# Optimization experiments

Hardware: AMD Instinct MI355X
Metric: run time of the kernel (lower is better)

## Reference

```python
import jax, jax.numpy as jnp
import numpy as np

SCORE_THR = 0.05
IOU_THR = 0.5
TOPK = 1000  # per-class candidate cap (static shape for jit)


def _make_anchors(img):
    """RetinaNet anchors: 9 per location over P3-P7 (strides 8..128)."""
    strides = [8, 16, 32, 64, 128]
    sizes = [32, 64, 128, 256, 512]
    ratios = [0.5, 1.0, 2.0]
    scales = [2.0 ** 0, 2.0 ** (1.0 / 3.0), 2.0 ** (2.0 / 3.0)]
    out = []
    for stride, size in zip(strides, sizes):
        ws, hs = [], []
        for r in ratios:
            for sc in scales:
                a = (size * sc) ** 2
                w = np.sqrt(a / r)
                ws.append(w)
                hs.append(w * r)
        ws = np.asarray(ws)
        hs = np.asarray(hs)
        fs = img // stride
        c = (np.arange(fs) + 0.5) * stride
        cy, cx = np.meshgrid(c, c, indexing='ij')
        cx = cx.reshape(-1)[:, None]
        cy = cy.reshape(-1)[:, None]
        boxes = np.stack([cx - ws / 2, cy - hs / 2, cx + ws / 2, cy + hs / 2], axis=-1)
        out.append(boxes.reshape(-1, 4))
    return np.concatenate(out, axis=0).astype(np.float32)


def setup_inputs() -> dict:
    key = jax.random.key(0)
    k1, k2 = jax.random.split(key)
    img = 1024
    anchors = jnp.asarray(_make_anchors(img))          # [196416, 4]
    A = anchors.shape[0]
    cls_heads = jax.random.uniform(k1, (1, A, 80), dtype=jnp.float32)   # post-sigmoid probs
    reg_heads = jax.random.normal(k2, (1, A, 4), dtype=jnp.float32)
    return {"cls_heads": cls_heads, "reg_heads": reg_heads, "anchors": anchors,
            "img_h": img, "img_w": img}


def _decode(anchors, deltas):
    # BBoxTransform: std = [0.1, 0.1, 0.2, 0.2]
    w = anchors[:, 2] - anchors[:, 0]
    h = anchors[:, 3] - anchors[:, 1]
    cx = anchors[:, 0] + 0.5 * w
    cy = anchors[:, 1] + 0.5 * h
    dx = deltas[:, 0] * 0.1
    dy = deltas[:, 1] * 0.1
    dw = deltas[:, 2] * 0.2
    dh = deltas[:, 3] * 0.2
    pcx = cx + dx * w
    pcy = cy + dy * h
    pw = jnp.exp(dw) * w
    ph = jnp.exp(dh) * h
    return jnp.stack([pcx - 0.5 * pw, pcy - 0.5 * ph,
                      pcx + 0.5 * pw, pcy + 0.5 * ph], axis=-1)


def _iou(b):  # [K,4] -> [K,K]
    area = jnp.maximum(b[:, 2] - b[:, 0], 0) * jnp.maximum(b[:, 3] - b[:, 1], 0)
    lt = jnp.maximum(b[:, None, :2], b[None, :, :2])
    rb = jnp.minimum(b[:, None, 2:], b[None, :, 2:])
    wh = jnp.maximum(rb - lt, 0.0)
    inter = wh[..., 0] * wh[..., 1]
    union = area[:, None] + area[None, :] - inter
    return inter / jnp.maximum(union, 1e-8)


def _nms_one_class(scores_c, boxes):
    # threshold, take top-K candidates (static shape), greedy NMS
    masked = jnp.where(scores_c > SCORE_THR, scores_c, -1.0)
    _, idx = jax.lax.top_k(masked, TOPK)
    s = scores_c[idx]                       # [K]
    b = boxes[idx]                          # [K,4]
    valid = s > SCORE_THR
    iou = _iou(b)                           # [K,K]
    rng = jnp.arange(TOPK)

    def body(i, keep):
        sup = (iou[i] > IOU_THR) & (rng > i) & keep[i]
        return keep & ~sup

    keep = jax.lax.fori_loop(0, TOPK, body, valid)
    return jnp.where(keep, s, 0.0), jnp.where(keep[:, None], b, 0.0), keep


def reference(cls_heads, reg_heads, anchors, img_h, img_w):
    # batch = 1 (the torch code squeezes the batch dim)
    scores_ac = cls_heads[0]                # [A, C]
    deltas = reg_heads[0]                   # [A, 4]
    boxes = _decode(anchors, deltas)        # [A, 4]
    # ClipBoxes
    boxes = jnp.stack([
        jnp.clip(boxes[:, 0], 0.0, img_w),
        jnp.clip(boxes[:, 1], 0.0, img_h),
        jnp.clip(boxes[:, 2], 0.0, img_w),
        jnp.clip(boxes[:, 3], 0.0, img_h)], axis=-1)
    scores_ca = scores_ac.T                 # [C, A]
    s, b, keep = jax.vmap(_nms_one_class, in_axes=(0, None))(scores_ca, boxes)
    C = scores_ca.shape[0]
    cls_idx = jnp.where(keep, jnp.arange(C)[:, None], -1)
    # padded, static-shape equivalent of (finalScores, finalAnchorBoxesIndexes,
    # finalAnchorBoxesCoordinates); invalid slots have score 0 / class -1
    return s.reshape(-1), cls_idx.reshape(-1), b.reshape(-1, 4)
```

## Files before the change

kernel.cpp:

```cpp
#include <hip/hip_runtime.h>
#include <hip/hip_bf16.h>
#include <math.h>

typedef unsigned long long u64;
typedef unsigned int u32;

#define C_NUM 80
#define TOPK 1000
#define CAP 2048
#define HB 128
#define STG 32
#define NCHUNK 16
#define SCORE_THR 0.05f
#define IOU_THR 0.5f
#define GRID_SCAN 256

__device__ __forceinline__ float exp_cr(float x) {
    return (float)exp((double)x);
}

__device__ __forceinline__ void decode_box(const float* __restrict__ anch,
                                           const float* __restrict__ reg,
                                           int a, float fw, float fh, float4* out) {
#pragma clang fp contract(off)
    float a0 = anch[(size_t)a * 4 + 0], a1 = anch[(size_t)a * 4 + 1];
    float a2 = anch[(size_t)a * 4 + 2], a3 = anch[(size_t)a * 4 + 3];
    float d0 = reg[(size_t)a * 4 + 0], d1 = reg[(size_t)a * 4 + 1];
    float d2 = reg[(size_t)a * 4 + 2], d3 = reg[(size_t)a * 4 + 3];
    float w = a2 - a0, h = a3 - a1;
    float cx = a0 + 0.5f * w, cy = a1 + 0.5f * h;
    float dx = d0 * 0.1f, dy = d1 * 0.1f, dw = d2 * 0.2f, dh = d3 * 0.2f;
    float t1 = dx * w; float pcx = cx + t1;
    float t2 = dy * h; float pcy = cy + t2;
    float pw = exp_cr(dw) * w;
    float ph = exp_cr(dh) * h;
    float x1 = pcx - 0.5f * pw, y1 = pcy - 0.5f * ph;
    float x2 = pcx + 0.5f * pw, y2 = pcy + 0.5f * ph;
    x1 = fminf(fmaxf(x1, 0.0f), fw);
    y1 = fminf(fmaxf(y1, 0.0f), fh);
    x2 = fminf(fmaxf(x2, 0.0f), fw);
    y2 = fminf(fmaxf(y2, 0.0f), fh);
    *out = make_float4(x1, y1, x2, y2);
}

__global__ __launch_bounds__(1024)
void hist_kernel(const float4* __restrict__ cls4, u32* __restrict__ slices, int nvec) {
    __shared__ u32 h[C_NUM * HB];
    int tid = threadIdx.x;
    for (int i = tid; i < C_NUM * HB; i += 1024) h[i] = 0u;
    __syncthreads();
    int gid = blockIdx.x * 1024 + tid;
    const int stride = GRID_SCAN * 1024;
    const int dC = (stride * 4) % C_NUM;
    int c0 = (gid * 4) % C_NUM;
    for (int v = gid; v < nvec; v += stride) {
        float4 f = cls4[v];
        float e[4] = {f.x, f.y, f.z, f.w};
        int cc = c0;
#pragma unroll
        for (int k = 0; k < 4; ++k) {
            int t = (((int)__float_as_uint(e[k])) - 0x3F000000) >> 16;
            if (t > 0) {
                t = t > HB - 1 ? HB - 1 : t;
                atomicAdd(&h[cc * HB + t], 1u);
            }
            cc++; if (cc == C_NUM) cc = 0;
        }
        c0 += dC; if (c0 >= C_NUM) c0 -= C_NUM;
    }
    __syncthreads();
    u32* my = slices + (size_t)blockIdx.x * (C_NUM * HB);
    for (int i = tid; i < C_NUM * HB; i += 1024) my[i] = h[i];
}

__global__ __launch_bounds__(1024)
void thr_kernel(const u32* __restrict__ slices, u32* __restrict__ thrG) {
    __shared__ u32 part[8][HB];
    __shared__ u32 s[HB];
    __shared__ int bsel;
    int c = blockIdx.x, tid = threadIdx.x;
    int b = tid & (HB - 1), g = tid >> 7;
    u32 sum = 0;
    const u32* base = slices + c * HB + b;
    for (int sl = g * 32; sl < g * 32 + 32; ++sl)
        sum += base[(size_t)sl * (C_NUM * HB)];
    part[g][b] = sum;
    if (tid == 0) bsel = 0;
    __syncthreads();
    if (tid < HB) {
        u32 t = 0;
#pragma unroll
        for (int g2 = 0; g2 < 8; ++g2) t += part[g2][tid];
        s[tid] = t;
    }
    __syncthreads();
    for (int d = 1; d < HB; d <<= 1) {
        u32 v = 0;
        if (tid < HB) v = s[tid] + ((tid + d < HB) ? s[tid + d] : 0u);
        __syncthreads();
        if (tid < HB) s[tid] = v;
        __syncthreads();
    }
    if (tid < HB) {
        u32 me = s[tid];
        u32 nxt = (tid < HB - 1) ? s[tid + 1] : 0u;
        if (me >= (u32)TOPK && (tid == HB - 1 || nxt < (u32)TOPK)) bsel = tid;
    }
    __syncthreads();
    if (tid == 0) {
        int bb = bsel;
        thrG[c] = (bb == 0) ? 0u : (u32)(0x3F000000 + (bb << 16));
    }
}

__global__ __launch_bounds__(1024)
void gather_kernel(const float4* __restrict__ cls4, const u32* __restrict__ thrG,
                   u32* __restrict__ cntG, u64* __restrict__ pool, int nvec) {
    __shared__ int thrS[C_NUM];
    __shared__ u32 lcnt[C_NUM];
    __shared__ u32 lbase[C_NUM];
    __shared__ u64 stage[C_NUM * STG];
    int tid = threadIdx.x;
    if (tid < C_NUM) { thrS[tid] = (int)thrG[tid]; lcnt[tid] = 0u; }
    __syncthreads();

    int gid = blockIdx.x * 1024 + tid;
    const int stride = GRID_SCAN * 1024;
    const int dA = (stride * 4) / C_NUM;
    const int dC = (stride * 4) % C_NUM;
    int base = gid * 4;
    int aa0 = base / C_NUM;
    int c0 = base - aa0 * C_NUM;
    for (int v = gid; v < nvec; v += stride) {
        float4 f = cls4[v];
        float e[4] = {f.x, f.y, f.z, f.w};
        int cc = c0, aa = aa0;
#pragma unroll
        for (int k = 0; k < 4; ++k) {
            int bits = (int)__float_as_uint(e[k]);
            if (bits >= thrS[cc]) {
                u64 key = ((u64)(u32)bits << 32) | (u64)(u32)(~(u32)aa);
                u32 p = atomicAdd(&lcnt[cc], 1u);
                if (p < STG) stage[cc * STG + p] = key;
                else {
                    u32 q = atomicAdd(&cntG[cc], 1u);
                    if (q < CAP) pool[(size_t)cc * CAP + q] = key;
                }
            }
            cc++; if (cc == C_NUM) { cc = 0; aa++; }
        }
        c0 += dC;
        if (c0 >= C_NUM) { c0 -= C_NUM; aa0 += dA + 1; } else aa0 += dA;
    }
    __syncthreads();
    if (tid < C_NUM) {
        u32 nl = lcnt[tid]; if (nl > STG) nl = STG;
        lbase[tid] = nl ? atomicAdd(&cntG[tid], nl) : 0u;
        lcnt[tid] = nl;
    }
    __syncthreads();
    for (int i = tid; i < C_NUM * STG; i += 1024) {
        int c = i >> 5, k = i & (STG - 1);
        if ((u32)k < lcnt[c]) {
            u32 q = lbase[c] + (u32)k;
            if (q < CAP) pool[(size_t)c * CAP + q] = stage[i];
        }
    }
}

__global__ __launch_bounds__(256)
void rank_kernel(const u64* __restrict__ pool, const u32* __restrict__ cntG,
                 const float* __restrict__ anchors, const float* __restrict__ regs,
                 const int* __restrict__ imh, const int* __restrict__ imw,
                 u64* __restrict__ sortedKey, float4* __restrict__ candBox,
                 float* __restrict__ candArea) {
    __shared__ __align__(16) u64 keys[CAP];
    int c = blockIdx.x, q = blockIdx.y, tid = threadIdx.x;
    int n = (int)cntG[c]; if (n > CAP) n = CAP;
    int my = q * 256 + tid;
    if (my >= n && my < TOPK) {
        int g = c * TOPK + my;
        sortedKey[g] = 0ull;
        candBox[g] = make_float4(0.f, 0.f, 0.f, 0.f);
        candArea[g] = 0.f;
    }
    if (q * 256 >= n) return;
    for (int i = tid; i < n; i += 256) keys[i] = pool[(size_t)c * CAP + i];
    __syncthreads();
    u64 k0 = (my < n) ? keys[my] : ~0ull;
    int r0 = 0;
    int j = 0;
    for (; j + 8 <= n; j += 8) {
        ulonglong2 p0 = *(const ulonglong2*)&keys[j];
        ulonglong2 p1 = *(const ulonglong2*)&keys[j + 2];
        ulonglong2 p2 = *(const ulonglong2*)&keys[j + 4];
        ulonglong2 p3 = *(const ulonglong2*)&keys[j + 6];
        r0 += (int)(p0.x > k0) + (int)(p0.y > k0)
            + (int)(p1.x > k0) + (int)(p1.y > k0)
            + (int)(p2.x > k0) + (int)(p2.y > k0)
            + (int)(p3.x > k0) + (int)(p3.y > k0);
    }
    for (; j < n; ++j) r0 += (int)(keys[j] > k0);
    if (my < n && r0 < TOPK) {
        float sc = __uint_as_float((u32)(k0 >> 32));
        int a = (int)(~(u32)k0);
        float fw = (float)(*imw), fh = (float)(*imh);
        float4 bx = make_float4(0.f, 0.f, 0.f, 0.f);
        if (sc > SCORE_THR) decode_box(anchors, regs, a, fw, fh, &bx);
        int g = c * TOPK + r0;
        sortedKey[g] = k0;
        candBox[g] = bx;
        candArea[g] = fmaxf(bx.z - bx.x, 0.0f) * fmaxf(bx.w - bx.y, 0.0f);
    }
}

__global__ __launch_bounds__(256)
void iou_kernel(const float4* __restrict__ candBox, const float* __restrict__ candArea,
                u64* __restrict__ supT) {
#pragma clang fp contract(off)
    __shared__ float4 box[NCHUNK * 64];
    __shared__ float area[NCHUNK * 64];
    int c = blockIdx.x, q = blockIdx.y;
    int tid = threadIdx.x, lane = tid & 63, wave = tid >> 6;
    int rowBase = q << 6;
    for (int i = rowBase + tid; i < NCHUNK * 64; i += 256) {
        if (i < TOPK) {
            box[i] = candBox[(size_t)c * TOPK + i];
            area[i] = candArea[(size_t)c * TOPK + i];
        } else {
            box[i] = make_float4(0.f, 0.f, 0.f, 0.f);
            area[i] = 0.f;
        }
    }
    __syncthreads();

    int rowEnd = TOPK - rowBase; if (rowEnd > 64) rowEnd = 64;
    const double CC = 0.5 + 0x1p-25;
    u64* colBase = supT + (size_t)c * (NCHUNK * 1024) + rowBase;

    for (int jw = q + wave; jw < NCHUNK; jw += 4) {
        int j = (jw << 6) | lane;
        float4 bj = box[j];
        float aj = area[j];
        u64 vw = 0ull;
#pragma unroll 8
        for (int r = 0; r < 64; ++r) {
            int i = rowBase + r;
            float4 bi = box[i];
            float ai = area[i];
            float ltx = fmaxf(bi.x, bj.x), lty = fmaxf(bi.y, bj.y);
            float rbx = fminf(bi.z, bj.z), rby = fminf(bi.w, bj.w);
            float ww = fmaxf(rbx - ltx, 0.0f), hh = fmaxf(rby - lty, 0.0f);
            float inter = ww * hh;
            float uni = (ai + aj) - inter;
            float d = fmaxf(uni, 1e-8f);
            bool sup = (double)inter > CC * (double)d;
            u64 w64 = __ballot(sup);
            if (jw == q) w64 &= (((~0ull) << 1) << r);
            vw = (lane == r) ? w64 : vw;
        }
        if (lane < rowEnd) colBase[(size_t)jw * 1024 + lane] = vw;
    }
}

__global__ __launch_bounds__(1024)
void nmsout_kernel(const u64* __restrict__ supT, const u64* __restrict__ sortedKey,
                   const float4* __restrict__ candBox, float* __restrict__ out) {
    __shared__ __align__(16) u64 supLds[NCHUNK * 1024];
    __shared__ u64 km[NCHUNK];
    __shared__ u64 maskArr[NCHUNK * 64];
    __shared__ int changed;
    int c = blockIdx.x, tid = threadIdx.x;
    int lane = tid & 63, wave = tid >> 6;

    const u64* base = supT + (size_t)c * (NCHUNK * 1024);
#pragma unroll
    for (int jw = 0; jw < NCHUNK; ++jw) {
        int R = (jw + 1) << 6; if (R > TOPK) R = TOPK;
        for (int i = tid; i < R; i += 1024)
            supLds[jw * 1024 + i] = base[(size_t)jw * 1024 + i];
    }

    u64 key = (tid < TOPK) ? sortedKey[c * TOPK + tid] : 0ull;
    float sc = __uint_as_float((u32)(key >> 32));
    bool valid = (tid < TOPK) && (sc > SCORE_THR);
    u64 kwValid = __ballot(valid);
    if (lane == 0) km[wave] = kwValid;
    if (tid == 0) changed = 1;
    __syncthreads();

    while (changed) {
        maskArr[tid] = 0ull - ((km[wave] >> lane) & 1ull);
        __syncthreads();
        if (tid == 0) changed = 0;
        u64 acc = 0ull;
        int R = (wave + 1) << 6;
        for (int i = lane; i < R; i += 64)
            acc |= supLds[wave * 1024 + i] & maskArr[i];
        u32 lo = (u32)acc, hi = (u32)(acc >> 32);
#pragma unroll
        for (int s = 1; s < 64; s <<= 1) {
            lo |= __shfl_xor(lo, s);
            hi |= __shfl_xor(hi, s);
        }
        u64 nk = kwValid & ~(((u64)hi << 32) | lo);
        __syncthreads();
        if (lane == 0) {
            if (nk != km[wave]) changed = 1;
            km[wave] = nk;
        }
        __syncthreads();
    }

    u64 kw = km[wave];
    if (tid < TOPK) {
        bool keep = (kw >> lane) & 1ull;
        int g = c * TOPK + tid;
        out[g] = keep ? sc : 0.0f;
        out[C_NUM * TOPK + g] = keep ? (float)c : -1.0f;
        float4 b = keep ? candBox[(size_t)c * TOPK + tid]
                        : make_float4(0.f, 0.f, 0.f, 0.f);
        ((float4*)(out + 2 * C_NUM * TOPK))[g] = b;
    }
}

extern "C" void kernel_launch(void* const* d_in, const int* in_sizes, int n_in,
                              void* d_out, int out_size, void* d_ws, size_t ws_size,
                              hipStream_t stream) {
    const float* cls  = (const float*)d_in[0];
    const float* reg  = (const float*)d_in[1];
    const float* anch = (const float*)d_in[2];
    const int* imh    = (const int*)d_in[3];
    const int* imw    = (const int*)d_in[4];
    int A = in_sizes[2] / 4;
    int nvec = (A * C_NUM) / 4;

    char* w = (char*)d_ws;
    size_t off = 0;
    auto alloc = [&](size_t bytes) -> void* {
        off = (off + 255) & ~(size_t)255;
        void* p = w + off;
        off += bytes;
        return p;
    };
    u32*    cntG      = (u32*)   alloc((size_t)C_NUM * 4);
    u32*    thrG      = (u32*)   alloc((size_t)C_NUM * 4);
    u32*    slices    = (u32*)   alloc((size_t)GRID_SCAN * C_NUM * HB * 4);
    u64*    pool      = (u64*)   alloc((size_t)C_NUM * CAP * 8);
    u64*    sortedKey = (u64*)   alloc((size_t)C_NUM * TOPK * 8);
    float4* candBox   = (float4*)alloc((size_t)C_NUM * TOPK * 16);
    float*  candArea  = (float*) alloc((size_t)C_NUM * TOPK * 4);
    u64*    supT      = (u64*)   alloc((size_t)C_NUM * NCHUNK * 1024 * 8);

    hipMemsetAsync(cntG, 0, (size_t)C_NUM * 4, stream);
    hist_kernel<<<GRID_SCAN, 1024, 0, stream>>>((const float4*)cls, slices, nvec);
    thr_kernel<<<C_NUM, 1024, 0, stream>>>(slices, thrG);
    gather_kernel<<<GRID_SCAN, 1024, 0, stream>>>((const float4*)cls, thrG, cntG, pool, nvec);
    rank_kernel<<<dim3(C_NUM, 8), 256, 0, stream>>>(pool, cntG, anch, reg, imh, imw,
                                                    sortedKey, candBox, candArea);
    iou_kernel<<<dim3(C_NUM, NCHUNK), 256, 0, stream>>>(candBox, candArea, supT);
    nmsout_kernel<<<C_NUM, 1024, 0, stream>>>(supT, sortedKey, candBox, (float*)d_out);
}
```

Baseline: 122.6 us.

## Rebalance IoU bitmask work per wave, drop memset, use float threshold compare

The IoU kernel now assigns each wave a balanced pair of column chunks within the upper-triangular (row, column) chunk space. It uses 9 blocks of 512 threads per class instead of 16 uneven blocks of 256, and each block loads the whole candidate set into LDS once. The double-precision threshold compare is replaced by a float compare (2*inter > union), and the separate memset of the class counters is folded into the histogram kernel. Together these aim to cut load imbalance, redundant LDS fills, FP64 work and one launch. The float compare may differ from the reference's rounding at exact-threshold boundaries.

After: 107.1 us. -12.7%, faster.

```diff
diff --git a/kernel.cpp b/kernel.cpp
--- a/kernel.cpp
+++ b/kernel.cpp
@@ -44,9 +44,11 @@
 }
 
 __global__ __launch_bounds__(1024)
-void hist_kernel(const float4* __restrict__ cls4, u32* __restrict__ slices, int nvec) {
+void hist_kernel(const float4* __restrict__ cls4, u32* __restrict__ slices,
+                 u32* __restrict__ cntG, int nvec) {
     __shared__ u32 h[C_NUM * HB];
     int tid = threadIdx.x;
+    if (blockIdx.x == 0 && tid < C_NUM) cntG[tid] = 0u;
     for (int i = tid; i < C_NUM * HB; i += 1024) h[i] = 0u;
     __syncthreads();
     int gid = blockIdx.x * 1024 + tid;
@@ -214,16 +216,15 @@
     }
 }
 
-__global__ __launch_bounds__(256)
+__global__ __launch_bounds__(512)
 void iou_kernel(const float4* __restrict__ candBox, const float* __restrict__ candArea,
                 u64* __restrict__ supT) {
 #pragma clang fp contract(off)
     __shared__ float4 box[NCHUNK * 64];
     __shared__ float area[NCHUNK * 64];
-    int c = blockIdx.x, q = blockIdx.y;
+    int c = blockIdx.x, bq = blockIdx.y;
     int tid = threadIdx.x, lane = tid & 63, wave = tid >> 6;
-    int rowBase = q << 6;
-    for (int i = rowBase + tid; i < NCHUNK * 64; i += 256) {
+    for (int i = tid; i < NCHUNK * 64; i += 512) {
         if (i < TOPK) {
             box[i] = candBox[(size_t)c * TOPK + i];
             area[i] = candArea[(size_t)c * TOPK + i];
@@ -234,32 +235,52 @@
     }
     __syncthreads();
 
+    int wid = bq * 8 + wave;
+    int q = 0, rem = wid;
+    while (rem >= ((17 - q) >> 1)) { rem -= (17 - q) >> 1; ++q; }
+    int jwA = q + 2 * rem;
+    int jwB = jwA + 1;
+    bool hasB = (jwB < NCHUNK);
+    bool diag = (rem == 0);
+
+    int rowBase = q << 6;
+    int jA = (jwA << 6) | lane;
+    int jB = hasB ? ((jwB << 6) | lane) : jA;
+    float4 bjA = box[jA]; float ajA = area[jA];
+    float4 bjB = box[jB]; float ajB = area[jB];
+    u64 vwA = 0ull, vwB = 0ull;
+
+#pragma unroll 16
+    for (int r = 0; r < 64; ++r) {
+        int i = rowBase + r;
+        float4 bi = box[i];
+        float ai = area[i];
+        float ltxA = fmaxf(bi.x, bjA.x), ltyA = fmaxf(bi.y, bjA.y);
+        float rbxA = fminf(bi.z, bjA.z), rbyA = fminf(bi.w, bjA.w);
+        float wwA = fmaxf(rbxA - ltxA, 0.0f), hhA = fmaxf(rbyA - ltyA, 0.0f);
+        float interA = wwA * hhA;
+        float dA = fmaxf((ai + ajA) - interA, 1e-8f);
+        bool supA = (interA + interA) > dA;
+        float ltxB = fmaxf(bi.x, bjB.x), ltyB = fmaxf(bi.y, bjB.y);
+        float rbxB = fminf(bi.z, bjB.z), rbyB = fminf(bi.w, bjB.w);
+        float wwB = fmaxf(rbxB - ltxB, 0.0f), hhB = fmaxf(rbyB - ltyB, 0.0f);
+        float interB = wwB * hhB;
+        float dB = fmaxf((ai + ajB) - interB, 1e-8f);
+        bool supB = (interB + interB) > dB;
+
+        u64 wA = __ballot(supA);
+        u64 wB = __ballot(supB);
+        if (diag) wA &= (((~0ull) << 1) << r);
+        bool sel = (lane == r);
+        vwA = sel ? wA : vwA;
+        vwB = sel ? wB : vwB;
+    }
+
     int rowEnd = TOPK - rowBase; if (rowEnd > 64) rowEnd = 64;
-    const double CC = 0.5 + 0x1p-25;
-    u64* colBase = supT + (size_t)c * (NCHUNK * 1024) + rowBase;
-
-    for (int jw = q + wave; jw < NCHUNK; jw += 4) {
-        int j = (jw << 6) | lane;
-        float4 bj = box[j];
-        float aj = area[j];
-        u64 vw = 0ull;
-#pragma unroll 8
-        for (int r = 0; r < 64; ++r) {
-            int i = rowBase + r;
-            float4 bi = box[i];
-            float ai = area[i];
-            float ltx = fmaxf(bi.x, bj.x), lty = fmaxf(bi.y, bj.y);
-            float rbx = fminf(bi.z, bj.z), rby = fminf(bi.w, bj.w);
-            float ww = fmaxf(rbx - ltx, 0.0f), hh = fmaxf(rby - lty, 0.0f);
-            float inter = ww * hh;
-            float uni = (ai + aj) - inter;
-            float d = fmaxf(uni, 1e-8f);
-            bool sup = (double)inter > CC * (double)d;
-            u64 w64 = __ballot(sup);
-            if (jw == q) w64 &= (((~0ull) << 1) << r);
-            vw = (lane == r) ? w64 : vw;
-        }
-        if (lane < rowEnd) colBase[(size_t)jw * 1024 + lane] = vw;
+    u64* clsBase = supT + (size_t)c * (NCHUNK * 1024);
+    if (lane < rowEnd) {
+        clsBase[(size_t)jwA * 1024 + rowBase + lane] = vwA;
+        if (hasB) clsBase[(size_t)jwB * 1024 + rowBase + lane] = vwB;
     }
 }
 
@@ -352,12 +373,11 @@
     float*  candArea  = (float*) alloc((size_t)C_NUM * TOPK * 4);
     u64*    supT      = (u64*)   alloc((size_t)C_NUM * NCHUNK * 1024 * 8);
 
-    hipMemsetAsync(cntG, 0, (size_t)C_NUM * 4, stream);
-    hist_kernel<<<GRID_SCAN, 1024, 0, stream>>>((const float4*)cls, slices, nvec);
+    hist_kernel<<<GRID_SCAN, 1024, 0, stream>>>((const float4*)cls, slices, cntG, nvec);
     thr_kernel<<<C_NUM, 1024, 0, stream>>>(slices, thrG);
     gather_kernel<<<GRID_SCAN, 1024, 0, stream>>>((const float4*)cls, thrG, cntG, pool, nvec);
     rank_kernel<<<dim3(C_NUM, 8), 256, 0, stream>>>(pool, cntG, anch, reg, imh, imw,
                                                     sortedKey, candBox, candArea);
-    iou_kernel<<<dim3(C_NUM, NCHUNK), 256, 0, stream>>>(candBox, candArea, supT);
+    iou_kernel<<<dim3(C_NUM, 9), 512, 0, stream>>>(candBox, candArea, supT);
     nmsout_kernel<<<C_NUM, 1024, 0, stream>>>(supT, sortedKey, candBox, (float*)d_out);
 }
```
